# Performance work log

Hardware: AMD Instinct MI355X
Metric: run time of the kernel (lower is better)

The kernel has to match this reference:

```python
import jax, jax.numpy as jnp
import numpy as np

B, S, D = 2, 2048, 1024
H = 16
HD = D // H

def setup_inputs() -> dict:
    key = jax.random.key(0)
    ks = jax.random.split(key, 9)
    s = 1.0 / np.sqrt(D)
    return {
        "x": jax.random.normal(ks[0], (B, S, D), dtype=jnp.float32),
        "Wq": jax.random.normal(ks[1], (D, D), dtype=jnp.float32) * s,
        "bq": jnp.zeros((D,), dtype=jnp.float32),
        "Wk": jax.random.normal(ks[2], (D, D), dtype=jnp.float32) * s,
        "bk": jnp.zeros((D,), dtype=jnp.float32),
        "Wv": jax.random.normal(ks[3], (D, D), dtype=jnp.float32) * s,
        "bv": jnp.zeros((D,), dtype=jnp.float32),
        "Wo": jax.random.normal(ks[4], (D, D), dtype=jnp.float32) * s,
        "bo": jnp.zeros((D,), dtype=jnp.float32),
    }

def reference(x, Wq, bq, Wk, bk, Wv, bv, Wo, bo):
    b, s, d = x.shape
    # torch Linear: y = x @ W.T + b
    def proj(W, bias):
        y = jnp.einsum('bsd,ed->bse', x, W) + bias
        return y.reshape(b, s, H, HD).transpose(0, 2, 1, 3)  # [b,h,s,hd]
    Q = proj(Wq, bq)
    K = proj(Wk, bk)
    V = proj(Wv, bv)
    scale = 1.0 / jnp.sqrt(jnp.float32(HD))
    scores = jnp.einsum('bhqd,bhkd->bhqk', Q, K) * scale  # [b,h,s,s]
    attn = jax.nn.softmax(scores, axis=-1)
    out = jnp.einsum('bhqk,bhkd->bhqd', attn, V)  # [b,h,s,hd]
    out = out.transpose(0, 2, 1, 3).reshape(b, s, d)
    return jnp.einsum('bsd,ed->bse', out, Wo) + bo
```

## Files before the change

### kernel.cpp

```cpp
#include <hip/hip_runtime.h>
#include <stdint.h>


typedef __bf16 bf16x8 __attribute__((ext_vector_type(8)));
typedef float  f32x4  __attribute__((ext_vector_type(4)));
typedef unsigned int u32x4v __attribute__((ext_vector_type(4)));

#define LOG2E 1.44269504088896f
#define FIXED_MAX_BITS 14.4269504088896f

__device__ __forceinline__ unsigned short f2bf(float f) {
    union { float f; unsigned u; } v; v.f = f;
    unsigned r = v.u + 0x7FFFu + ((v.u >> 16) & 1u);
    return (unsigned short)(r >> 16);
}
__device__ __forceinline__ float bf2f(unsigned short u) {
    union { unsigned u; float f; } v; v.u = (unsigned)u << 16; return v.f;
}

__device__ __forceinline__ unsigned cvtpk(float a, float b) {
#if __has_builtin(__builtin_amdgcn_cvt_pk_bf16_f32)
    return __builtin_bit_cast(unsigned, __builtin_amdgcn_cvt_pk_bf16_f32(a, b));
#else
    return (unsigned)f2bf(a) | ((unsigned)f2bf(b) << 16);
#endif
}

__device__ __forceinline__ float exp2_fast(float x) {
#if __has_builtin(__builtin_amdgcn_exp2f)
    return __builtin_amdgcn_exp2f(x);
#else
    return __expf(x * 0.69314718056f);
#endif
}

__device__ __forceinline__ void glds16(const void* g, void* l) {
    __builtin_amdgcn_global_load_lds(
        (__attribute__((address_space(1))) void*)(g),
        (__attribute__((address_space(3))) void*)(l),
        16, 0, 0);
}

__global__ __launch_bounds__(256) void cvt_all(
    const float* __restrict__ x,  const float* __restrict__ Wq,
    const float* __restrict__ Wk, const float* __restrict__ Wv,
    const float* __restrict__ Wo,
    unsigned short* __restrict__ xb,  unsigned short* __restrict__ Wqb,
    unsigned short* __restrict__ Wkb, unsigned short* __restrict__ Wvb,
    unsigned short* __restrict__ Wob)
{
    const int stride = gridDim.x * blockDim.x;
    for (int i = blockIdx.x * blockDim.x + threadIdx.x; i < 2097152; i += stride) {
        const float* src; unsigned short* dst; int j;
        if (i < 1048576) { src = x; dst = xb; j = i; }
        else {
            int t = (i - 1048576) >> 18; j = (i - 1048576) & 262143;
            src = (t == 0) ? Wq : (t == 1) ? Wk : (t == 2) ? Wv : Wo;
            dst = (t == 0) ? Wqb : (t == 1) ? Wkb : (t == 2) ? Wvb : Wob;
        }
        float4 v = ((const float4*)src)[j];
        uint2 o;
        o.x = cvtpk(v.x, v.y);
        o.y = cvtpk(v.z, v.w);
        ((uint2*)dst)[j] = o;
    }
}

template <int MODE>
__global__ __launch_bounds__(256) void gemm_bt(
    const unsigned short* __restrict__ A,
    const unsigned short* __restrict__ W0,
    const unsigned short* __restrict__ W1,
    const unsigned short* __restrict__ W2,
    const float* __restrict__ b0,
    const float* __restrict__ b1,
    const float* __restrict__ b2,
    unsigned short* __restrict__ outQ,
    unsigned short* __restrict__ outK,
    unsigned short* __restrict__ outV,
    float* __restrict__ outF)
{
    constexpr int BM = (MODE == 0) ? 128 : 64;
    constexpr int FM = BM / 32;
    constexpr int RA = BM / 32;

    __shared__ __attribute__((aligned(16))) unsigned short As[BM * 64];
    __shared__ __attribute__((aligned(16))) unsigned short Bs[128 * 64];

    const int tid  = threadIdx.x;
    const int lane = tid & 63;
    const int wid  = tid >> 6;
    const int quad = lane >> 4;
    const int l16  = lane & 15;

    const int m0 = blockIdx.x * BM;

    const unsigned short* W;
    const float* bias;
    int proj, n0;
    if (MODE == 0) {
        proj = blockIdx.y >> 3;
        n0   = (blockIdx.y & 7) * 128;
        W    = (proj == 0) ? W0 : (proj == 1) ? W1 : W2;
        bias = (proj == 0) ? b0 : (proj == 1) ? b1 : b2;
    } else {
        proj = 0;
        n0   = blockIdx.y * 128;
        W    = W0;
        bias = b0;
    }

    const int wm = (wid >> 1) * (BM / 2);
    const int wn = (wid & 1) * 64;

    f32x4 acc[FM][4];
#pragma unroll
    for (int i = 0; i < FM; ++i)
#pragma unroll
        for (int j = 0; j < 4; ++j)
            acc[i][j] = (f32x4){0.f, 0.f, 0.f, 0.f};

    char* AsB  = (char*)As;
    char* BsB  = (char*)Bs;
    char* ldsA = AsB + wid * 1024;
    char* ldsB = BsB + wid * 1024;

    for (int k0 = 0; k0 < 1024; k0 += 64) {
#pragma unroll
        for (int q = 0; q < RA; ++q) {
            int i   = q * 256 + tid;
            int row = i >> 3;
            int sc  = (i & 7) ^ (row & 7);
            glds16(A + (size_t)(m0 + row) * 1024 + k0 + sc * 8, ldsA + q * 4096);
        }
#pragma unroll
        for (int q = 0; q < 4; ++q) {
            int i   = q * 256 + tid;
            int row = i >> 3;
            int sc  = (i & 7) ^ (row & 7);
            glds16(W + (size_t)(n0 + row) * 1024 + k0 + sc * 8, ldsB + q * 4096);
        }
        __syncthreads();

#pragma unroll
        for (int kh = 0; kh < 2; ++kh) {
            bf16x8 af[FM], bfr[4];
#pragma unroll
            for (int t = 0; t < FM; ++t) {
                int r = wm + t * 16 + l16;
                int c = (kh * 4 + quad) ^ (r & 7);
                af[t] = *(const bf16x8*)(AsB + r * 128 + c * 16);
            }
#pragma unroll
            for (int t = 0; t < 4; ++t) {
                int r = wn + t * 16 + l16;
                int c = (kh * 4 + quad) ^ (r & 7);
                bfr[t] = *(const bf16x8*)(BsB + r * 128 + c * 16);
            }
#pragma unroll
            for (int i = 0; i < FM; ++i)
#pragma unroll
                for (int j = 0; j < 4; ++j)
                    acc[i][j] = __builtin_amdgcn_mfma_f32_16x16x32_bf16(
                        af[i], bfr[j], acc[i][j], 0, 0, 0);
        }
        __syncthreads();
    }

#pragma unroll
    for (int i = 0; i < FM; ++i) {
        const int mrow0 = m0 + wm + i * 16 + quad * 4;
#pragma unroll
        for (int j = 0; j < 4; ++j) {
            const int n  = n0 + wn + j * 16 + l16;
            const float bb = bias[n];
            if (MODE == 1) {
#pragma unroll
                for (int r = 0; r < 4; ++r)
                    outF[(size_t)(mrow0 + r) * 1024 + n] = acc[i][j][r] + bb;
            } else {
                const int h = n >> 6, hd = n & 63;
                if (proj == 2) {
                    const int b = mrow0 >> 11, s = mrow0 & 2047;
                    uint2 pk;
                    pk.x = cvtpk(acc[i][j][0] + bb, acc[i][j][1] + bb);
                    pk.y = cvtpk(acc[i][j][2] + bb, acc[i][j][3] + bb);
                    *(uint2*)(outV + ((size_t)((b * 16 + h) * 64 + hd)) * 2048 + s) = pk;
                } else {
                    unsigned short* dst = (proj == 0) ? outQ : outK;
                    const float scl = (proj == 0) ? (0.125f * LOG2E) : 1.0f;
#pragma unroll
                    for (int r = 0; r < 4; ++r) {
                        const int m = mrow0 + r;
                        const int b = m >> 11, s = m & 2047;
                        dst[((size_t)((b * 16 + h) * 2048 + s)) * 64 + hd] =
                            f2bf((acc[i][j][r] + bb) * scl);
                    }
                }
            }
        }
    }
}

__global__ __launch_bounds__(128, 8) void attn_kernel(
    const unsigned short* __restrict__ Qb,
    const unsigned short* __restrict__ Kb,
    const unsigned short* __restrict__ Vtb,
    unsigned short* __restrict__ OP,
    float* __restrict__ LS)
{
    __shared__ __attribute__((aligned(16))) unsigned short Ks[64 * 64];
    __shared__ __attribute__((aligned(16))) unsigned short Vs[64 * 64];

    const int tid  = threadIdx.x;
    const int lane = tid & 63;
    const int wid  = tid >> 6;
    const int quad = lane >> 4;
    const int l16  = lane & 15;
    const int l7   = l16 & 7;

    const int half = blockIdx.x & 1;
    const int q0   = (blockIdx.x >> 1) * 64 + wid * 32;
    const int hb   = blockIdx.y;
    const int bq   = hb >> 4, hh = hb & 15;

    const unsigned short* Qh  = Qb  + (size_t)hb * 2048 * 64;
    const unsigned short* Kh  = Kb  + (size_t)hb * 2048 * 64;
    const unsigned short* Vth = Vtb + (size_t)hb * 64 * 2048;

    bf16x8 qf[2][2];
#pragma unroll
    for (int qt = 0; qt < 2; ++qt) {
        const unsigned short* qp = Qh + (size_t)(q0 + qt * 16 + l16) * 64 + quad * 8;
        qf[qt][0] = *(const bf16x8*)(qp);
        qf[qt][1] = *(const bf16x8*)(qp + 32);
    }

    f32x4 o[4][2];
#pragma unroll
    for (int ht = 0; ht < 4; ++ht)
#pragma unroll
        for (int qt = 0; qt < 2; ++qt)
            o[ht][qt] = (f32x4){0.f, 0.f, 0.f, 0.f};
    float lsum[2] = {0.f, 0.f};

    char* KsB = (char*)Ks;
    char* VsB = (char*)Vs;
    char* ldsK = KsB + wid * 1024;
    char* ldsV = VsB + wid * 1024;

    const int base_row = 8 * (l16 >> 2) + (l16 & 3);
    const int kp0 = ((quad) ^ l7) * 16;
    const int kp1 = ((4 + quad) ^ l7) * 16;
    const int vrow = l16 * 128;

    const int kc0 = half * 1024;
    for (int kc = kc0; kc < kc0 + 1024; kc += 64) {
#pragma unroll
        for (int q = 0; q < 4; ++q) {
            int i   = q * 128 + tid;
            int row = i >> 3;
            int g   = (row & 3) | (((row >> 3) & 1) << 2);
            int ch  = (i & 7) ^ g;
            glds16(Kh + (size_t)(kc + row) * 64 + ch * 8, ldsK + q * 2048);
        }
#pragma unroll
        for (int q = 0; q < 4; ++q) {
            int i   = q * 128 + tid;
            int row = i >> 3;
            int ch  = (i & 7) ^ (row & 7);
            glds16(Vth + (size_t)row * 2048 + kc + ch * 8, ldsV + q * 2048);
        }
        __syncthreads();

#pragma unroll
        for (int st32 = 0; st32 < 2; ++st32) {
            const char* krb = KsB + (st32 * 32 + base_row) * 128;
            bf16x8 kf00 = *(const bf16x8*)(krb + kp0);
            bf16x8 kf01 = *(const bf16x8*)(krb + kp1);
            bf16x8 kf10 = *(const bf16x8*)(krb + 512 + kp0);
            bf16x8 kf11 = *(const bf16x8*)(krb + 512 + kp1);

            const f32x4 mi = (f32x4){-FIXED_MAX_BITS, -FIXED_MAX_BITS,
                                     -FIXED_MAX_BITS, -FIXED_MAX_BITS};
            f32x4 s00 = mi, s01 = mi, s10 = mi, s11 = mi;
            s00 = __builtin_amdgcn_mfma_f32_16x16x32_bf16(kf00, qf[0][0], s00, 0, 0, 0);
            s00 = __builtin_amdgcn_mfma_f32_16x16x32_bf16(kf01, qf[0][1], s00, 0, 0, 0);
            s01 = __builtin_amdgcn_mfma_f32_16x16x32_bf16(kf10, qf[0][0], s01, 0, 0, 0);
            s01 = __builtin_amdgcn_mfma_f32_16x16x32_bf16(kf11, qf[0][1], s01, 0, 0, 0);
            s10 = __builtin_amdgcn_mfma_f32_16x16x32_bf16(kf00, qf[1][0], s10, 0, 0, 0);
            s10 = __builtin_amdgcn_mfma_f32_16x16x32_bf16(kf01, qf[1][1], s10, 0, 0, 0);
            s11 = __builtin_amdgcn_mfma_f32_16x16x32_bf16(kf10, qf[1][0], s11, 0, 0, 0);
            s11 = __builtin_amdgcn_mfma_f32_16x16x32_bf16(kf11, qf[1][1], s11, 0, 0, 0);

            bf16x8 p8[2];
#pragma unroll
            for (int qt = 0; qt < 2; ++qt) {
                const f32x4 sA = qt ? s10 : s00;
                const f32x4 sB = qt ? s11 : s01;
                float e0 = exp2_fast(sA[0]), e1 = exp2_fast(sA[1]);
                float e2 = exp2_fast(sA[2]), e3 = exp2_fast(sA[3]);
                float e4 = exp2_fast(sB[0]), e5 = exp2_fast(sB[1]);
                float e6 = exp2_fast(sB[2]), e7 = exp2_fast(sB[3]);
                lsum[qt] += ((e0 + e1) + (e2 + e3)) + ((e4 + e5) + (e6 + e7));
                u32x4v up;
                up.x = cvtpk(e0, e1);
                up.y = cvtpk(e2, e3);
                up.z = cvtpk(e4, e5);
                up.w = cvtpk(e6, e7);
                p8[qt] = __builtin_bit_cast(bf16x8, up);
            }

            const int voff = vrow + (((st32 * 4 + quad) ^ l7) * 16);
#pragma unroll
            for (int ht = 0; ht < 4; ++ht) {
                const bf16x8 vf = *(const bf16x8*)(VsB + voff + ht * 2048);
                o[ht][0] = __builtin_amdgcn_mfma_f32_16x16x32_bf16(vf, p8[0], o[ht][0], 0, 0, 0);
                o[ht][1] = __builtin_amdgcn_mfma_f32_16x16x32_bf16(vf, p8[1], o[ht][1], 0, 0, 0);
            }
        }
        __syncthreads();
    }

    float lt[2];
#pragma unroll
    for (int qt = 0; qt < 2; ++qt) {
        float s = lsum[qt];
        s += __shfl_xor(s, 16);
        s += __shfl_xor(s, 32);
        lt[qt] = s;
    }

    unsigned short* OPh = OP + (size_t)half * 4096 * 1024;
#pragma unroll
    for (int qt = 0; qt < 2; ++qt) {
        const size_t row = (size_t)(bq * 2048 + q0 + qt * 16 + l16);
#pragma unroll
        for (int ht = 0; ht < 4; ++ht) {
            uint2 pk;
            pk.x = cvtpk(o[ht][qt][0], o[ht][qt][1]);
            pk.y = cvtpk(o[ht][qt][2], o[ht][qt][3]);
            *(uint2*)(OPh + row * 1024 + hh * 64 + ht * 16 + quad * 4) = pk;
        }
    }
    if (quad == 0) {
        LS[half * 65536 + hb * 2048 + q0 + l16]      = lt[0];
        LS[half * 65536 + hb * 2048 + q0 + 16 + l16] = lt[1];
    }
}

__global__ __launch_bounds__(256) void attn_reduce(
    const unsigned short* __restrict__ OP,
    const float* __restrict__ LS,
    unsigned short* __restrict__ attnb)
{
    const size_t idx = ((size_t)blockIdx.x * 256 + threadIdx.x) * 8;
    const int row = (int)(idx >> 10);
    const int col = (int)(idx & 1023);
    const int bh  = ((row >> 11) << 4) + (col >> 6);
    const int q   = row & 2047;
    const float l = LS[bh * 2048 + q] + LS[65536 + bh * 2048 + q];
    const float rl = 1.0f / l;

    ushort4 a0 = *(const ushort4*)(OP + idx);
    ushort4 a1 = *(const ushort4*)(OP + idx + 4);
    ushort4 b0 = *(const ushort4*)(OP + 4194304 + idx);
    ushort4 b1 = *(const ushort4*)(OP + 4194304 + idx + 4);
    u32x4v o;
    o.x = cvtpk((bf2f(a0.x) + bf2f(b0.x)) * rl, (bf2f(a0.y) + bf2f(b0.y)) * rl);
    o.y = cvtpk((bf2f(a0.z) + bf2f(b0.z)) * rl, (bf2f(a0.w) + bf2f(b0.w)) * rl);
    o.z = cvtpk((bf2f(a1.x) + bf2f(b1.x)) * rl, (bf2f(a1.y) + bf2f(b1.y)) * rl);
    o.w = cvtpk((bf2f(a1.z) + bf2f(b1.z)) * rl, (bf2f(a1.w) + bf2f(b1.w)) * rl);
    *(u32x4v*)(attnb + idx) = o;
}

extern "C" void kernel_launch(void* const* d_in, const int* in_sizes, int n_in,
                              void* d_out, int out_size, void* d_ws, size_t ws_size,
                              hipStream_t stream) {
    (void)in_sizes; (void)n_in; (void)out_size; (void)ws_size;

    const float* x  = (const float*)d_in[0];
    const float* Wq = (const float*)d_in[1];
    const float* bq = (const float*)d_in[2];
    const float* Wk = (const float*)d_in[3];
    const float* bk = (const float*)d_in[4];
    const float* Wv = (const float*)d_in[5];
    const float* bv = (const float*)d_in[6];
    const float* Wo = (const float*)d_in[7];
    const float* bo = (const float*)d_in[8];

    char* ws = (char*)d_ws;
    const size_t MB = 1024 * 1024;
    unsigned short* xb    = (unsigned short*)(ws + 0);
    unsigned short* Wqb   = (unsigned short*)(ws + 8  * MB);
    unsigned short* Wkb   = (unsigned short*)(ws + 10 * MB);
    unsigned short* Wvb   = (unsigned short*)(ws + 12 * MB);
    unsigned short* Wob   = (unsigned short*)(ws + 14 * MB);
    unsigned short* Qb    = (unsigned short*)(ws + 16 * MB);
    unsigned short* Kb    = (unsigned short*)(ws + 24 * MB);
    unsigned short* Vtb   = (unsigned short*)(ws + 32 * MB);
    unsigned short* attnb = (unsigned short*)(ws + 40 * MB);
    unsigned short* OP    = (unsigned short*)(ws + 48 * MB);
    float*          LSb   = (float*)(ws + 64 * MB);

    cvt_all<<<dim3(1024), dim3(256), 0, stream>>>(
        x, Wq, Wk, Wv, Wo, xb, Wqb, Wkb, Wvb, Wob);

    gemm_bt<0><<<dim3(32, 24), dim3(256), 0, stream>>>(
        xb, Wqb, Wkb, Wvb, bq, bk, bv, Qb, Kb, Vtb, nullptr);

    attn_kernel<<<dim3(64, 32), dim3(128), 0, stream>>>(Qb, Kb, Vtb, OP, LSb);

    attn_reduce<<<dim3(2048), dim3(256), 0, stream>>>(OP, LSb, attnb);

    gemm_bt<1><<<dim3(64, 8), dim3(256), 0, stream>>>(
        attnb, Wob, nullptr, nullptr, bo, nullptr, nullptr,
        nullptr, nullptr, nullptr, (float*)d_out);
}
```

Measured before the change: 217.5 us.

## Split attention keys four ways with 256-thread blocks sharing K/V tiles

The attention kernel now runs 4 waves per block, each block covering 128 queries, so every K/V tile loaded into LDS is reused by twice as many queries. The key range is split into four 512-key chunks instead of two, keeping the grid size unchanged. The reduce kernel sums four partial outputs and four partial row sums, which adds partial-buffer traffic and workspace. The partial-sum buffer moves to a new workspace offset to make room for the larger partial-output buffer.

```diff
diff --git a/kernel.cpp b/kernel.cpp
--- a/kernel.cpp
+++ b/kernel.cpp
@@ -202,7 +202,7 @@
     }
 }
 
-__global__ __launch_bounds__(128, 8) void attn_kernel(
+__global__ __launch_bounds__(256, 8) void attn_kernel(
     const unsigned short* __restrict__ Qb,
     const unsigned short* __restrict__ Kb,
     const unsigned short* __restrict__ Vtb,
@@ -219,10 +219,10 @@
     const int l16  = lane & 15;
     const int l7   = l16 & 7;
 
-    const int half = blockIdx.x & 1;
-    const int q0   = (blockIdx.x >> 1) * 64 + wid * 32;
-    const int hb   = blockIdx.y;
-    const int bq   = hb >> 4, hh = hb & 15;
+    const int split = blockIdx.x & 3;
+    const int q0    = (blockIdx.x >> 2) * 128 + wid * 32;
+    const int hb    = blockIdx.y;
+    const int bq    = hb >> 4, hh = hb & 15;
 
     const unsigned short* Qh  = Qb  + (size_t)hb * 2048 * 64;
     const unsigned short* Kh  = Kb  + (size_t)hb * 2048 * 64;
@@ -254,22 +254,22 @@
     const int kp1 = ((4 + quad) ^ l7) * 16;
     const int vrow = l16 * 128;
 
-    const int kc0 = half * 1024;
-    for (int kc = kc0; kc < kc0 + 1024; kc += 64) {
-#pragma unroll
-        for (int q = 0; q < 4; ++q) {
-            int i   = q * 128 + tid;
+    const int kc0 = split * 512;
+    for (int kc = kc0; kc < kc0 + 512; kc += 64) {
+#pragma unroll
+        for (int q = 0; q < 2; ++q) {
+            int i   = q * 256 + tid;
             int row = i >> 3;
             int g   = (row & 3) | (((row >> 3) & 1) << 2);
             int ch  = (i & 7) ^ g;
-            glds16(Kh + (size_t)(kc + row) * 64 + ch * 8, ldsK + q * 2048);
-        }
-#pragma unroll
-        for (int q = 0; q < 4; ++q) {
-            int i   = q * 128 + tid;
+            glds16(Kh + (size_t)(kc + row) * 64 + ch * 8, ldsK + q * 4096);
+        }
+#pragma unroll
+        for (int q = 0; q < 2; ++q) {
+            int i   = q * 256 + tid;
             int row = i >> 3;
             int ch  = (i & 7) ^ (row & 7);
-            glds16(Vth + (size_t)row * 2048 + kc + ch * 8, ldsV + q * 2048);
+            glds16(Vth + (size_t)row * 2048 + kc + ch * 8, ldsV + q * 4096);
         }
         __syncthreads();
 
@@ -331,7 +331,7 @@
         lt[qt] = s;
     }
 
-    unsigned short* OPh = OP + (size_t)half * 4096 * 1024;
+    unsigned short* OPh = OP + (size_t)split * 4096 * 1024;
 #pragma unroll
     for (int qt = 0; qt < 2; ++qt) {
         const size_t row = (size_t)(bq * 2048 + q0 + qt * 16 + l16);
@@ -344,8 +344,8 @@
         }
     }
     if (quad == 0) {
-        LS[half * 65536 + hb * 2048 + q0 + l16]      = lt[0];
-        LS[half * 65536 + hb * 2048 + q0 + 16 + l16] = lt[1];
+        LS[split * 65536 + hb * 2048 + q0 + l16]      = lt[0];
+        LS[split * 65536 + hb * 2048 + q0 + 16 + l16] = lt[1];
     }
 }
 
@@ -359,18 +359,25 @@
     const int col = (int)(idx & 1023);
     const int bh  = ((row >> 11) << 4) + (col >> 6);
     const int q   = row & 2047;
-    const float l = LS[bh * 2048 + q] + LS[65536 + bh * 2048 + q];
+    const int lsi = bh * 2048 + q;
+    const float l = (LS[lsi] + LS[65536 + lsi]) + (LS[131072 + lsi] + LS[196608 + lsi]);
     const float rl = 1.0f / l;
 
-    ushort4 a0 = *(const ushort4*)(OP + idx);
-    ushort4 a1 = *(const ushort4*)(OP + idx + 4);
-    ushort4 b0 = *(const ushort4*)(OP + 4194304 + idx);
-    ushort4 b1 = *(const ushort4*)(OP + 4194304 + idx + 4);
+    float acc[8] = {0.f, 0.f, 0.f, 0.f, 0.f, 0.f, 0.f, 0.f};
+#pragma unroll
+    for (int p = 0; p < 4; ++p) {
+        ushort4 a0 = *(const ushort4*)(OP + (size_t)p * 4194304 + idx);
+        ushort4 a1 = *(const ushort4*)(OP + (size_t)p * 4194304 + idx + 4);
+        acc[0] += bf2f(a0.x); acc[1] += bf2f(a0.y);
+        acc[2] += bf2f(a0.z); acc[3] += bf2f(a0.w);
+        acc[4] += bf2f(a1.x); acc[5] += bf2f(a1.y);
+        acc[6] += bf2f(a1.z); acc[7] += bf2f(a1.w);
+    }
     u32x4v o;
-    o.x = cvtpk((bf2f(a0.x) + bf2f(b0.x)) * rl, (bf2f(a0.y) + bf2f(b0.y)) * rl);
-    o.y = cvtpk((bf2f(a0.z) + bf2f(b0.z)) * rl, (bf2f(a0.w) + bf2f(b0.w)) * rl);
-    o.z = cvtpk((bf2f(a1.x) + bf2f(b1.x)) * rl, (bf2f(a1.y) + bf2f(b1.y)) * rl);
-    o.w = cvtpk((bf2f(a1.z) + bf2f(b1.z)) * rl, (bf2f(a1.w) + bf2f(b1.w)) * rl);
+    o.x = cvtpk(acc[0] * rl, acc[1] * rl);
+    o.y = cvtpk(acc[2] * rl, acc[3] * rl);
+    o.z = cvtpk(acc[4] * rl, acc[5] * rl);
+    o.w = cvtpk(acc[6] * rl, acc[7] * rl);
     *(u32x4v*)(attnb + idx) = o;
 }
 
@@ -401,7 +408,7 @@
     unsigned short* Vtb   = (unsigned short*)(ws + 32 * MB);
     unsigned short* attnb = (unsigned short*)(ws + 40 * MB);
     unsigned short* OP    = (unsigned short*)(ws + 48 * MB);
-    float*          LSb   = (float*)(ws + 64 * MB);
+    float*          LSb   = (float*)(ws + 80 * MB);
 
     cvt_all<<<dim3(1024), dim3(256), 0, stream>>>(
         x, Wq, Wk, Wv, Wo, xb, Wqb, Wkb, Wvb, Wob);
@@ -409,7 +416,7 @@
     gemm_bt<0><<<dim3(32, 24), dim3(256), 0, stream>>>(
         xb, Wqb, Wkb, Wvb, bq, bk, bv, Qb, Kb, Vtb, nullptr);
 
-    attn_kernel<<<dim3(64, 32), dim3(128), 0, stream>>>(Qb, Kb, Vtb, OP, LSb);
+    attn_kernel<<<dim3(64, 32), dim3(256), 0, stream>>>(Qb, Kb, Vtb, OP, LSb);
 
     attn_reduce<<<dim3(2048), dim3(256), 0, stream>>>(OP, LSb, attnb);
 
```

After: 560.2 us. +157.6%, slower.

## Enlarge attention tiles to 128 queries/keys and compute row sums via MFMA

Applied to the files above, without the earlier changes.

The attention kernel now uses 256-thread blocks covering 128 query rows, and each iteration loads 128 keys into doubled K/V shared buffers, halving the number of barriers and sharing each K/V tile across more waves. The scalar exp-sum accumulation and cross-lane shuffles are replaced by an extra MFMA against a vector of bf16 ones, which yields the softmax denominator from the same bf16-rounded probabilities used in P·V. This trades VALU work for extra matrix instructions and raises LDS use per block, which may reduce occupancy.

```diff
diff --git a/kernel.cpp b/kernel.cpp
--- a/kernel.cpp
+++ b/kernel.cpp
@@ -202,15 +202,15 @@
     }
 }
 
-__global__ __launch_bounds__(128, 8) void attn_kernel(
+__global__ __launch_bounds__(256, 4) void attn_kernel(
     const unsigned short* __restrict__ Qb,
     const unsigned short* __restrict__ Kb,
     const unsigned short* __restrict__ Vtb,
     unsigned short* __restrict__ OP,
     float* __restrict__ LS)
 {
-    __shared__ __attribute__((aligned(16))) unsigned short Ks[64 * 64];
-    __shared__ __attribute__((aligned(16))) unsigned short Vs[64 * 64];
+    __shared__ __attribute__((aligned(16))) unsigned short Ks[128 * 64];
+    __shared__ __attribute__((aligned(16))) unsigned short Vs[2 * 64 * 64];
 
     const int tid  = threadIdx.x;
     const int lane = tid & 63;
@@ -220,7 +220,7 @@
     const int l7   = l16 & 7;
 
     const int half = blockIdx.x & 1;
-    const int q0   = (blockIdx.x >> 1) * 64 + wid * 32;
+    const int q0   = (blockIdx.x >> 1) * 128 + wid * 32;
     const int hb   = blockIdx.y;
     const int bq   = hb >> 4, hh = hb & 15;
 
@@ -236,18 +236,19 @@
         qf[qt][1] = *(const bf16x8*)(qp + 32);
     }
 
+    const u32x4v ones_u = (u32x4v){0x3F803F80u, 0x3F803F80u, 0x3F803F80u, 0x3F803F80u};
+    const bf16x8 ones8  = __builtin_bit_cast(bf16x8, ones_u);
+
     f32x4 o[4][2];
 #pragma unroll
     for (int ht = 0; ht < 4; ++ht)
 #pragma unroll
         for (int qt = 0; qt < 2; ++qt)
             o[ht][qt] = (f32x4){0.f, 0.f, 0.f, 0.f};
-    float lsum[2] = {0.f, 0.f};
-
-    char* KsB = (char*)Ks;
-    char* VsB = (char*)Vs;
+    f32x4 o4[2] = {(f32x4){0.f, 0.f, 0.f, 0.f}, (f32x4){0.f, 0.f, 0.f, 0.f}};
+
+    char* KsB  = (char*)Ks;
     char* ldsK = KsB + wid * 1024;
-    char* ldsV = VsB + wid * 1024;
 
     const int base_row = 8 * (l16 >> 2) + (l16 & 3);
     const int kp0 = ((quad) ^ l7) * 16;
@@ -255,26 +256,29 @@
     const int vrow = l16 * 128;
 
     const int kc0 = half * 1024;
-    for (int kc = kc0; kc < kc0 + 1024; kc += 64) {
+    for (int kc = kc0; kc < kc0 + 1024; kc += 128) {
 #pragma unroll
         for (int q = 0; q < 4; ++q) {
-            int i   = q * 128 + tid;
+            int i   = q * 256 + tid;
             int row = i >> 3;
             int g   = (row & 3) | (((row >> 3) & 1) << 2);
             int ch  = (i & 7) ^ g;
-            glds16(Kh + (size_t)(kc + row) * 64 + ch * 8, ldsK + q * 2048);
-        }
-#pragma unroll
-        for (int q = 0; q < 4; ++q) {
-            int i   = q * 128 + tid;
-            int row = i >> 3;
-            int ch  = (i & 7) ^ (row & 7);
-            glds16(Vth + (size_t)row * 2048 + kc + ch * 8, ldsV + q * 2048);
-        }
+            glds16(Kh + (size_t)(kc + row) * 64 + ch * 8, ldsK + q * 4096);
+        }
+#pragma unroll
+        for (int sub = 0; sub < 2; ++sub)
+#pragma unroll
+            for (int q = 0; q < 2; ++q) {
+                int i   = q * 256 + tid;
+                int row = i >> 3;
+                int ch  = (i & 7) ^ (row & 7);
+                glds16(Vth + (size_t)row * 2048 + kc + sub * 64 + ch * 8,
+                       (char*)Vs + sub * 8192 + wid * 1024 + q * 4096);
+            }
         __syncthreads();
 
 #pragma unroll
-        for (int st32 = 0; st32 < 2; ++st32) {
+        for (int st32 = 0; st32 < 4; ++st32) {
             const char* krb = KsB + (st32 * 32 + base_row) * 128;
             bf16x8 kf00 = *(const bf16x8*)(krb + kp0);
             bf16x8 kf01 = *(const bf16x8*)(krb + kp1);
@@ -298,37 +302,26 @@
             for (int qt = 0; qt < 2; ++qt) {
                 const f32x4 sA = qt ? s10 : s00;
                 const f32x4 sB = qt ? s11 : s01;
-                float e0 = exp2_fast(sA[0]), e1 = exp2_fast(sA[1]);
-                float e2 = exp2_fast(sA[2]), e3 = exp2_fast(sA[3]);
-                float e4 = exp2_fast(sB[0]), e5 = exp2_fast(sB[1]);
-                float e6 = exp2_fast(sB[2]), e7 = exp2_fast(sB[3]);
-                lsum[qt] += ((e0 + e1) + (e2 + e3)) + ((e4 + e5) + (e6 + e7));
                 u32x4v up;
-                up.x = cvtpk(e0, e1);
-                up.y = cvtpk(e2, e3);
-                up.z = cvtpk(e4, e5);
-                up.w = cvtpk(e6, e7);
+                up.x = cvtpk(exp2_fast(sA[0]), exp2_fast(sA[1]));
+                up.y = cvtpk(exp2_fast(sA[2]), exp2_fast(sA[3]));
+                up.z = cvtpk(exp2_fast(sB[0]), exp2_fast(sB[1]));
+                up.w = cvtpk(exp2_fast(sB[2]), exp2_fast(sB[3]));
                 p8[qt] = __builtin_bit_cast(bf16x8, up);
             }
 
-            const int voff = vrow + (((st32 * 4 + quad) ^ l7) * 16);
+            const int voff = (st32 >> 1) * 8192 + vrow
+                           + ((((st32 & 1) * 4 + quad) ^ l7) * 16);
 #pragma unroll
             for (int ht = 0; ht < 4; ++ht) {
-                const bf16x8 vf = *(const bf16x8*)(VsB + voff + ht * 2048);
+                const bf16x8 vf = *(const bf16x8*)((char*)Vs + voff + ht * 2048);
                 o[ht][0] = __builtin_amdgcn_mfma_f32_16x16x32_bf16(vf, p8[0], o[ht][0], 0, 0, 0);
                 o[ht][1] = __builtin_amdgcn_mfma_f32_16x16x32_bf16(vf, p8[1], o[ht][1], 0, 0, 0);
             }
+            o4[0] = __builtin_amdgcn_mfma_f32_16x16x32_bf16(ones8, p8[0], o4[0], 0, 0, 0);
+            o4[1] = __builtin_amdgcn_mfma_f32_16x16x32_bf16(ones8, p8[1], o4[1], 0, 0, 0);
         }
         __syncthreads();
-    }
-
-    float lt[2];
-#pragma unroll
-    for (int qt = 0; qt < 2; ++qt) {
-        float s = lsum[qt];
-        s += __shfl_xor(s, 16);
-        s += __shfl_xor(s, 32);
-        lt[qt] = s;
     }
 
     unsigned short* OPh = OP + (size_t)half * 4096 * 1024;
@@ -344,8 +337,8 @@
         }
     }
     if (quad == 0) {
-        LS[half * 65536 + hb * 2048 + q0 + l16]      = lt[0];
-        LS[half * 65536 + hb * 2048 + q0 + 16 + l16] = lt[1];
+        LS[half * 65536 + hb * 2048 + q0 + l16]      = o4[0][0];
+        LS[half * 65536 + hb * 2048 + q0 + 16 + l16] = o4[1][0];
     }
 }
 
@@ -359,7 +352,8 @@
     const int col = (int)(idx & 1023);
     const int bh  = ((row >> 11) << 4) + (col >> 6);
     const int q   = row & 2047;
-    const float l = LS[bh * 2048 + q] + LS[65536 + bh * 2048 + q];
+    const int lsi = bh * 2048 + q;
+    const float l = LS[lsi] + LS[65536 + lsi];
     const float rl = 1.0f / l;
 
     ushort4 a0 = *(const ushort4*)(OP + idx);
@@ -409,7 +403,7 @@
     gemm_bt<0><<<dim3(32, 24), dim3(256), 0, stream>>>(
         xb, Wqb, Wkb, Wvb, bq, bk, bv, Qb, Kb, Vtb, nullptr);
 
-    attn_kernel<<<dim3(64, 32), dim3(128), 0, stream>>>(Qb, Kb, Vtb, OP, LSb);
+    attn_kernel<<<dim3(32, 32), dim3(256), 0, stream>>>(Qb, Kb, Vtb, OP, LSb);
 
     attn_reduce<<<dim3(2048), dim3(256), 0, stream>>>(OP, LSb, attnb);
 
```

New measurement: 199.8 us. 1.09x faster.
